# Performance work log

Measured on AMD Instinct MI355X. Metric: run time of the kernel, lower is better.

## Reference

```python
import jax, jax.numpy as jnp
import numpy as np

HIDDEN = 450
DEPTH = 8
VOCAB = 780
N_NODES = 5120
N_MESS = 10241


def setup_inputs() -> dict:
    key = jax.random.key(0)
    ks = jax.random.split(key, 16)
    s = 0.05  # weight scale for numerical sanity
    return {
        "fnode": jax.random.randint(ks[0], (N_NODES,), 0, VOCAB),
        "fmess": jax.random.randint(ks[1], (N_MESS,), 0, N_NODES),
        "node_graph": jax.random.randint(ks[2], (N_NODES, 6), 0, N_MESS),
        "mess_graph": jax.random.randint(ks[3], (N_MESS, 5), 0, N_MESS),
        "emb": jax.random.normal(ks[4], (VOCAB, HIDDEN), jnp.float32),
        "Wz": jax.random.normal(ks[5], (2 * HIDDEN, HIDDEN), jnp.float32) * s,
        "bz": jnp.zeros((HIDDEN,), jnp.float32),
        "Wr": jax.random.normal(ks[6], (HIDDEN, HIDDEN), jnp.float32) * s,
        "Ur": jax.random.normal(ks[7], (HIDDEN, HIDDEN), jnp.float32) * s,
        "bu": jnp.zeros((HIDDEN,), jnp.float32),
        "Wh": jax.random.normal(ks[8], (2 * HIDDEN, HIDDEN), jnp.float32) * s,
        "bh": jnp.zeros((HIDDEN,), jnp.float32),
        "Wo": jax.random.normal(ks[9], (2 * HIDDEN, HIDDEN), jnp.float32) * s,
        "bo": jnp.zeros((HIDDEN,), jnp.float32),
        "batch_size": 128,
    }


def _gru(fmess_e, mess_graph, Wz, bz, Wr, Ur, bu, Wh, bh):
    # JTNN graph-GRU: depth-unrolled message updates over the message graph.
    M = fmess_e.shape[0]
    h0 = jnp.zeros((M, HIDDEN), fmess_e.dtype)
    mask = jnp.ones((M, 1), fmess_e.dtype).at[0].set(0.0)  # slot 0 = dummy message
    r1 = (fmess_e @ Wr)[:, None, :]  # loop-invariant W_r(fmess), [M,1,H]

    def step(h, _):
        h_nei = h[mess_graph]                     # [M,K,H] gather (index_select_ND)
        sum_h = h_nei.sum(axis=1)                 # [M,H]
        z = jax.nn.sigmoid(jnp.concatenate([fmess_e, sum_h], -1) @ Wz + bz)
        r = jax.nn.sigmoid(r1 + h_nei @ Ur + bu)  # [M,K,H]
        sum_gh = (r * h_nei).sum(axis=1)
        pre_h = jnp.tanh(jnp.concatenate([fmess_e, sum_gh], -1) @ Wh + bh)
        h = ((1.0 - z) * sum_h + z * pre_h) * mask
        return h, None

    h, _ = jax.lax.scan(step, h0, None, length=DEPTH)
    return h


def reference(fnode, fmess, node_graph, mess_graph, emb, Wz, bz, Wr, Ur, bu,
              Wh, bh, Wo, bo, batch_size):
    x = emb[fnode]                    # [N,H] embedding gather
    fmess_e = x[fmess]                # [M,H] message input features
    h = _gru(fmess_e, mess_graph, Wz, bz, Wr, Ur, bu, Wh, bh)  # [M,H]
    mess_nei = h[node_graph]          # [N,Kn,H]
    node_vecs = jnp.concatenate([x, mess_nei.sum(axis=1)], -1)  # [N,2H]
    node_vecs = jax.nn.relu(node_vecs @ Wo + bo)                # outputNN
    # uniform scope: every tree has N_NODES // batch_size nodes -> static reshape
    tree_vecs = node_vecs.reshape(batch_size, -1, HIDDEN)       # [B,L,H]
    messages = jnp.zeros((mess_graph.shape[0], HIDDEN), node_vecs.dtype)
    return (tree_vecs, messages)
```

## Files before the change

kernel.cpp:

```cpp
#include <hip/hip_runtime.h>
#include <cstdint>
#include <cstddef>

#define H 450
#define H2 900
#define KP 480
#define KP2 960
#define NMESS 10241
#define NNODE 5120
#define MPAD 10368
#define SPP1 960
#define SPP2 1920
#define PPSZ ((size_t)MPAD * SPP1)
#define KM 5
#define KN 6
#define LDCH 960

typedef __attribute__((ext_vector_type(8))) short short8;
typedef __attribute__((ext_vector_type(4))) float f32x4;

__device__ __forceinline__ short bf16rne(float f) {
  union { float f; unsigned u; } x; x.f = f;
  unsigned u = x.u;
  u += 0x7FFF + ((u >> 16) & 1);
  return (short)(u >> 16);
}
__device__ __forceinline__ float bf16tof(short s) {
  union { float f; unsigned u; } x;
  x.u = ((unsigned)(unsigned short)s) << 16;
  return x.f;
}
__device__ __forceinline__ void bf16split(float v, short& hi, short& lo) {
  hi = bf16rne(v);
  lo = bf16rne(v - bf16tof(hi));
}
__device__ __forceinline__ float sigmoidf_(float x) {
  return 1.f / (1.f + __expf(-x));
}

__device__ __forceinline__ size_t ppix(int row, int k, int spp) {
  return (size_t)row * spp + ((k >> 5) << 6) + (k & 31);
}

__device__ __forceinline__ void gll16(const short* g, short* l) {
  __builtin_amdgcn_global_load_lds(
      (const __attribute__((address_space(1))) void*)g,
      (__attribute__((address_space(3))) void*)l, 16, 0, 0);
}

#define BM 64
#define BN 64
#define BK 32

struct SmemT { short As[2][64][64]; short Bs[2][64][64]; };

__device__ __forceinline__ void xcd_swz(int gx, int gy, int& bm, int& bn) {
  const int nwg = gx * gy;
  int lid = blockIdx.y * gx + blockIdx.x;
  const int q = nwg >> 3, r = nwg & 7;
  const int xcd = lid & 7, seq = lid >> 3;
  int sid = (xcd < r) ? (xcd * (q + 1) + seq)
                      : (r * (q + 1) + (xcd - r) * q + seq);
  bm = (sid / gx) * BM;
  bn = (sid % gx) * BN;
}

template<int ACT, int OUT>
__device__ __forceinline__ void gemm_core(
    SmemT& sm, const short* __restrict__ Apk, int Kpad,
    const short* __restrict__ Bpk,
    const float* __restrict__ bias,
    float* C, int ldc, short* Cs,
    int M, int N, int bm, int bn)
{
  const int tid  = threadIdx.x;
  const int lane = tid & 63;
  const int wid  = tid >> 6;
  const int wm   = (wid >> 1) * 32;
  const int wn   = (wid & 1) * 32;
  const int l15  = lane & 15;
  const int s8   = (lane >> 4) * 8;
  const int rr0  = (lane >> 4) * 4;
  const int spp  = Kpad * 2;

  const int lr = lane >> 3;
  const int sl = lane & 7;
  const int t0 = sl ^ lr;
  const short* src[4];
#pragma unroll
  for (int qq = 0; qq < 4; ++qq) {
    const int rrow = wid * 32 + qq * 8 + lr;
    const bool isA = rrow < 64;
    const int grow = isA ? (bm + rrow) : (bn + rrow - 64);
    src[qq] = (isA ? Apk : Bpk) + (size_t)grow * spp + t0 * 8;
  }
  const int nk = Kpad / BK;

  f32x4 acc[2][2];
#pragma unroll
  for (int i = 0; i < 2; ++i)
#pragma unroll
    for (int j = 0; j < 2; ++j)
#pragma unroll
      for (int t = 0; t < 4; ++t) acc[i][j][t] = 0.f;

  auto STAGE = [&](int b, int koff) {
#pragma unroll
    for (int qq = 0; qq < 4; ++qq) {
      const int r0 = wid * 32 + qq * 8;
      short* d = (r0 < 64) ? &sm.As[b][r0][0] : &sm.Bs[b][r0 - 64][0];
      gll16(src[qq] + koff, d);
    }
  };

  STAGE(0, 0);
  __syncthreads();
  int cur = 0;
  for (int t = 0; t < nk; ++t) {
    if (t + 1 < nk) STAGE(cur ^ 1, (t + 1) * 64);
    short8 ah[2], al[2], bh[2], bl[2];
#pragma unroll
    for (int i = 0; i < 2; ++i) {
      const int rA = wm + i*16 + l15;
      const int xr = (rA & 7) << 3;
      ah[i] = *(const short8*)&sm.As[cur][rA][(s8)      ^ xr];
      al[i] = *(const short8*)&sm.As[cur][rA][(s8 + 32) ^ xr];
    }
#pragma unroll
    for (int j = 0; j < 2; ++j) {
      const int rB = wn + j*16 + l15;
      const int xr = (rB & 7) << 3;
      bh[j] = *(const short8*)&sm.Bs[cur][rB][(s8)      ^ xr];
      bl[j] = *(const short8*)&sm.Bs[cur][rB][(s8 + 32) ^ xr];
    }
    __builtin_amdgcn_s_setprio(1);
#pragma unroll
    for (int j = 0; j < 2; ++j)
#pragma unroll
      for (int i = 0; i < 2; ++i) {
        acc[i][j] = __builtin_amdgcn_mfma_f32_16x16x32_bf16(ah[i], bh[j], acc[i][j], 0, 0, 0);
        acc[i][j] = __builtin_amdgcn_mfma_f32_16x16x32_bf16(al[i], bh[j], acc[i][j], 0, 0, 0);
        acc[i][j] = __builtin_amdgcn_mfma_f32_16x16x32_bf16(ah[i], bl[j], acc[i][j], 0, 0, 0);
      }
    __builtin_amdgcn_s_setprio(0);
    __syncthreads();
    cur ^= 1;
  }

#pragma unroll
  for (int j = 0; j < 2; ++j) {
    int col = bn + wn + j*16 + l15;
    if (col >= N) continue;
    float bv = ((OUT == 0 || OUT == 3) && bias) ? bias[col] : 0.f;
#pragma unroll
    for (int i = 0; i < 2; ++i) {
      int row0 = bm + wm + i*16 + rr0;
#pragma unroll
      for (int rr = 0; rr < 4; ++rr) {
        int row = row0 + rr;
        if (row >= M) continue;
        float v = acc[i][j][rr] + bv;
        if (OUT == 0) {
          if (ACT == 1) v = fmaxf(v, 0.f);
          C[(size_t)row * ldc + col] = v;
        } else if (OUT == 1) {
          short hi, lo; bf16split(v, hi, lo);
          size_t o = ppix(row, col, SPP1);
          Cs[o] = hi; Cs[o + 32] = lo;
        } else {
          Cs[(size_t)row * ldc + col] = bf16rne(v);
        }
      }
    }
  }
}

template<int ACT>
__global__ __launch_bounds__(256, 5)
void gemm4(const short* __restrict__ Apk, int Kpad,
           const short* __restrict__ Bpk,
           const float* __restrict__ bias,
           float* C, int ldc, int M, int N)
{
  __shared__ SmemT sm;
  int bm, bn; xcd_swz(gridDim.x, gridDim.y, bm, bn);
  gemm_core<ACT, 0>(sm, Apk, Kpad, Bpk, bias, C, ldc, nullptr, M, N, bm, bn);
}

__global__ __launch_bounds__(256, 5)
void gemm4_b(const short* __restrict__ Apk, int Kpad,
             const short* __restrict__ Bpk,
             const float* __restrict__ bias,
             short* Cs, int ldcs, int M, int N)
{
  __shared__ SmemT sm;
  int bm, bn; xcd_swz(gridDim.x, gridDim.y, bm, bn);
  gemm_core<0, 3>(sm, Apk, Kpad, Bpk, bias, nullptr, ldcs, Cs, M, N, bm, bn);
}

__global__ __launch_bounds__(256, 5)
void gemm4_pair(const short* __restrict__ A0, const short* __restrict__ B0,
                float* C0,
                const short* __restrict__ A1, const short* __restrict__ B1,
                short* C1)
{
  __shared__ SmemT sm;
  int bm, bn; xcd_swz(gridDim.x, gridDim.y, bm, bn);
  if (blockIdx.z == 0)
    gemm_core<0, 0>(sm, A0, KP, B0, nullptr, C0, H, nullptr, NMESS, H, bm, bn);
  else
    gemm_core<0, 1>(sm, A1, KP, B1, nullptr, nullptr, 0, C1, NMESS, H, bm, bn);
}

__global__ __launch_bounds__(256)
void k_wT(const float* __restrict__ W, int Kreal,
          short* __restrict__ Bt, int Kpad, int rmax) {
  __shared__ float T[32][33];
  const int tx = threadIdx.x & 31;
  const int ty = threadIdx.x >> 5;
  const int k0 = blockIdx.x * 32;
  const int c0 = blockIdx.y * 32;
  const int spp = Kpad * 2;
#pragma unroll
  for (int i = 0; i < 4; ++i) {
    int k = k0 + ty + i*8, c = c0 + tx;
    T[ty + i*8][tx] = (k < Kreal && c < H) ? W[(size_t)k * H + c] : 0.f;
  }
  __syncthreads();
#pragma unroll
  for (int i = 0; i < 4; ++i) {
    int c = c0 + ty + i*8, k = k0 + tx;
    if (k < Kpad && c < rmax) {
      short hi, lo;
      bf16split(T[tx][ty + i*8], hi, lo);
      size_t o = ppix(c, k, spp);
      Bt[o] = hi; Bt[o + 32] = lo;
    }
  }
}

__global__ void k_biascat(const float* __restrict__ bz, const float* __restrict__ bh,
                          float* __restrict__ biasI) {
  int c = blockIdx.x * blockDim.x + threadIdx.x;
  if (c >= 900) return;
  biasI[c] = (c < 450) ? bz[c] : bh[c - 450];
}


__global__ void k_build_idx(const int* __restrict__ fnode,
                            const int* __restrict__ fmess,
                            int* __restrict__ idxM) {
  int m = blockIdx.x * blockDim.x + threadIdx.x;
  if (m < NMESS) idxM[m] = fnode[fmess[m]];
}

__global__ void k_embsplit(const float* __restrict__ emb,
                           const int* __restrict__ idxM,
                           short* __restrict__ eP) {
  int m = blockIdx.x, j = threadIdx.x * 2;
  if (j >= KP) return;
  size_t o = ppix(m, j, SPP1);
  if (j < H) {
    float2 v = *(const float2*)&emb[(size_t)idxM[m] * H + j];
    short2 h2, l2;
    bf16split(v.x, h2.x, l2.x); bf16split(v.y, h2.y, l2.y);
    *(short2*)&eP[o] = h2; *(short2*)&eP[o + 32] = l2;
  } else {
    short2 z2; z2.x = 0; z2.y = 0;
    *(short2*)&eP[o] = z2; *(short2*)&eP[o + 32] = z2;
  }
}

__global__ void k_h1(const short* __restrict__ CHb, short* __restrict__ hP) {
  int m = blockIdx.x, j = threadIdx.x * 2;
  if (j >= KP) return;
  size_t oP = ppix(m, j, SPP1);
  if (j < H) {
    size_t oc = (size_t)m * LDCH + j;
    short2 cz2 = *(const short2*)&CHb[oc];
    short2 ch2 = *(const short2*)&CHb[oc + 450];
    float v0 = sigmoidf_(bf16tof(cz2.x)) * tanhf(bf16tof(ch2.x));
    float v1 = sigmoidf_(bf16tof(cz2.y)) * tanhf(bf16tof(ch2.y));
    if (m == 0) { v0 = 0.f; v1 = 0.f; }
    short2 h2, l2;
    bf16split(v0, h2.x, l2.x); bf16split(v1, h2.y, l2.y);
    *(short2*)&hP[oP] = h2; *(short2*)&hP[oP + 32] = l2;
  } else {
    short2 z2; z2.x = 0; z2.y = 0;
    *(short2*)&hP[oP] = z2; *(short2*)&hP[oP + 32] = z2;
  }
}

__global__ void k_gather2(const short* __restrict__ hP,
                          const float* __restrict__ g,
                          const short* __restrict__ r1b,
                          const int* __restrict__ mg,
                          short* __restrict__ shP, short* __restrict__ ghP) {
  int m = blockIdx.x, j = threadIdx.x * 2;
  if (j >= KP) return;
  size_t o = ppix(m, j, SPP1);
  if (j >= H) {
    short2 z2; z2.x = 0; z2.y = 0;
    *(short2*)&shP[o] = z2; *(short2*)&shP[o + 32] = z2;
    *(short2*)&ghP[o] = z2; *(short2*)&ghP[o + 32] = z2;
    return;
  }
  const int* e = mg + (size_t)m * KM;
  short2 rb2 = *(const short2*)&r1b[(size_t)m * 480 + j];
  float rb0 = bf16tof(rb2.x), rb1 = bf16tof(rb2.y);
  float s0 = 0.f, s1 = 0.f, t0 = 0.f, t1 = 0.f;
#pragma unroll
  for (int k = 0; k < KM; ++k) {
    int ek = e[k];
    size_t oP = ppix(ek, j, SPP1);
    float2 gv = *(const float2*)&g[(size_t)ek * H + j];
    short2 ph = *(const short2*)&hP[oP];
    short2 pl = *(const short2*)&hP[oP + 32];
    float h0 = bf16tof(ph.x) + bf16tof(pl.x);
    float h1 = bf16tof(ph.y) + bf16tof(pl.y);
    s0 += h0;                          s1 += h1;
    t0 += sigmoidf_(rb0 + gv.x) * h0;  t1 += sigmoidf_(rb1 + gv.y) * h1;
  }
  short2 h2, l2;
  bf16split(s0, h2.x, l2.x); bf16split(s1, h2.y, l2.y);
  *(short2*)&shP[o] = h2; *(short2*)&shP[o + 32] = l2;
  bf16split(t0, h2.x, l2.x); bf16split(t1, h2.y, l2.y);
  *(short2*)&ghP[o] = h2; *(short2*)&ghP[o + 32] = l2;
}

__global__ void k_combine(const short* __restrict__ CHb,
                          const float* __restrict__ th,
                          const short* __restrict__ shP,
                          short* hP) {
  int m = blockIdx.x, j = threadIdx.x * 2;
  if (j >= KP) return;
  size_t oP = ppix(m, j, SPP1);
  if (j >= H) {
    short2 z2; z2.x = 0; z2.y = 0;
    *(short2*)&hP[oP] = z2; *(short2*)&hP[oP + 32] = z2;
    return;
  }
  size_t oc = (size_t)m * LDCH + j;
  size_t og = (size_t)m * H + j;
  short2 cz2 = *(const short2*)&CHb[oc];
  short2 ch2 = *(const short2*)&CHb[oc + 450];
  float2 tv  = *(const float2*)&th[og];
  short2 tzh = *(const short2*)&hP[oP];
  short2 tzl = *(const short2*)&hP[oP + 32];
  short2 smh = *(const short2*)&shP[oP];
  short2 sml = *(const short2*)&shP[oP + 32];
  float tz0 = bf16tof(tzh.x) + bf16tof(tzl.x);
  float tz1 = bf16tof(tzh.y) + bf16tof(tzl.y);
  float sm0 = bf16tof(smh.x) + bf16tof(sml.x);
  float sm1 = bf16tof(smh.y) + bf16tof(sml.y);
  float z0 = sigmoidf_(bf16tof(cz2.x) + tz0);
  float z1 = sigmoidf_(bf16tof(cz2.y) + tz1);
  float p0 = tanhf(bf16tof(ch2.x) + tv.x);
  float p1 = tanhf(bf16tof(ch2.y) + tv.y);
  float v0 = (1.f - z0) * sm0 + z0 * p0;
  float v1 = (1.f - z1) * sm1 + z1 * p1;
  if (m == 0) { v0 = 0.f; v1 = 0.f; }
  short2 h2, l2;
  bf16split(v0, h2.x, l2.x); bf16split(v1, h2.y, l2.y);
  *(short2*)&hP[oP] = h2; *(short2*)&hP[oP + 32] = l2;
}

__global__ void k_nodecat(const float* __restrict__ emb,
                          const int* __restrict__ fnode,
                          const short* __restrict__ hP,
                          const int* __restrict__ ng,
                          short* __restrict__ Apk) {
  int n = blockIdx.x, t = threadIdx.x, j = t * 2;
  if (j < H) {
    float2 v = *(const float2*)&emb[(size_t)fnode[n] * H + j];
    short2 h2, l2;
    bf16split(v.x, h2.x, l2.x); bf16split(v.y, h2.y, l2.y);
    size_t o = ppix(n, j, SPP2);
    *(short2*)&Apk[o] = h2; *(short2*)&Apk[o + 32] = l2;

    const int* e = ng + (size_t)n * KN;
    float s0 = 0.f, s1 = 0.f;
#pragma unroll
    for (int k = 0; k < KN; ++k) {
      size_t oP = ppix(e[k], j, SPP1);
      short2 ph = *(const short2*)&hP[oP];
      short2 pl = *(const short2*)&hP[oP + 32];
      s0 += bf16tof(ph.x) + bf16tof(pl.x);
      s1 += bf16tof(ph.y) + bf16tof(pl.y);
    }
    bf16split(s0, h2.x, l2.x); bf16split(s1, h2.y, l2.y);
    o = ppix(n, 450 + j, SPP2);
    *(short2*)&Apk[o] = h2; *(short2*)&Apk[o + 32] = l2;
  }
  if (t < 30) {
    int c = 900 + t * 2;
    short2 z2; z2.x = 0; z2.y = 0;
    size_t o = ppix(n, c, SPP2);
    *(short2*)&Apk[o] = z2; *(short2*)&Apk[o + 32] = z2;
  }
}


extern "C" void kernel_launch(void* const* d_in, const int* in_sizes, int n_in,
                              void* d_out, int out_size, void* d_ws, size_t ws_size,
                              hipStream_t stream) {
  (void)in_sizes; (void)n_in; (void)out_size; (void)ws_size;

  const int*   fnode      = (const int*)d_in[0];
  const int*   fmess      = (const int*)d_in[1];
  const int*   node_graph = (const int*)d_in[2];
  const int*   mess_graph = (const int*)d_in[3];
  const float* emb        = (const float*)d_in[4];
  const float* Wz         = (const float*)d_in[5];
  const float* bz         = (const float*)d_in[6];
  const float* Wr         = (const float*)d_in[7];
  const float* Ur         = (const float*)d_in[8];
  const float* bu         = (const float*)d_in[9];
  const float* Wh         = (const float*)d_in[10];
  const float* bh         = (const float*)d_in[11];
  const float* Wo         = (const float*)d_in[12];
  const float* bo         = (const float*)d_in[13];

  short* P   = (short*)d_ws;
  short* hP  = P;
  short* shP = P + 1 * PPSZ;
  short* ghP = P + 2 * PPSZ;
  short* CHb = P + 3 * PPSZ;
  float* g   = (float*)(CHb + (size_t)NMESS * LDCH + 64);
  short* r1b = (short*)(g + (size_t)NMESS * H);

  char*  scr  = (char*)d_out + (size_t)NNODE * H * 4;
  short* BtI  = (short*)scr;
  short* BtR  = BtI  + (size_t)1408 * SPP1;
  short* BtUr = BtR  + (size_t)512 * SPP1;
  short* BtZ  = BtUr + (size_t)512 * SPP1;
  short* BtHH = BtZ  + (size_t)512 * SPP1;
  short* BtO  = BtHH + (size_t)512 * SPP1;
  float* biasI = (float*)(BtO + (size_t)512 * SPP2);
  int*   idxM  = (int*)(biasI + 912);

  k_build_idx<<<(NMESS + 255) / 256, 256, 0, stream>>>(fnode, fmess, idxM);

  dim3 gT(KP / 32, 16), gT2(KP2 / 32, 16);
  k_wT<<<gT,  256, 0, stream>>>(Wz,                  H, BtI,               KP,  512);
  k_wT<<<gT,  256, 0, stream>>>(Wh,                  H, BtI + 450 * SPP1,  KP,  512);
  k_wT<<<gT,  256, 0, stream>>>(Wr,                  H, BtR,               KP,  512);
  k_wT<<<gT,  256, 0, stream>>>(Ur,                  H, BtUr,              KP,  512);
  k_wT<<<gT,  256, 0, stream>>>(Wz + (size_t)H * H,  H, BtZ,               KP,  512);
  k_wT<<<gT,  256, 0, stream>>>(Wh + (size_t)H * H,  H, BtHH,              KP,  512);
  k_wT<<<gT2, 256, 0, stream>>>(Wo,                 H2, BtO,               KP2, 512);
  k_biascat<<<4, 256, 0, stream>>>(bz, bh, biasI);

  k_embsplit<<<NMESS, 256, 0, stream>>>(emb, idxM, ghP);

  dim3 gI1(15, MPAD / BM);
  gemm4_b<<<gI1, 256, 0, stream>>>(ghP, KP, BtI, biasI, CHb, LDCH, NMESS, H2);
  dim3 gI2(8, MPAD / BM);
  gemm4_b<<<gI2, 256, 0, stream>>>(ghP, KP, BtR, bu, r1b, 480, NMESS, H);

  k_h1<<<NMESS, 256, 0, stream>>>(CHb, hP);

  dim3 gB(8, MPAD / BM);
  dim3 gP(8, MPAD / BM, 2);
  for (int d = 1; d < 8; ++d) {
    gemm4<0><<<gB, 256, 0, stream>>>(hP, KP, BtUr, nullptr, g, H, NMESS, H);
    k_gather2<<<NMESS, 256, 0, stream>>>(hP, g, r1b, mess_graph, shP, ghP);
    gemm4_pair<<<gP, 256, 0, stream>>>(ghP, BtHH, g, shP, BtZ, hP);
    k_combine<<<NMESS, 256, 0, stream>>>(CHb, g, shP, hP);
  }

  k_nodecat<<<NNODE, 256, 0, stream>>>(emb, fnode, hP, node_graph, shP);
  dim3 gF(8, NNODE / BM);
  gemm4<1><<<gF, 256, 0, stream>>>(shP, KP2, BtO, bo, (float*)d_out, H, NNODE, H);

  hipMemsetAsync((float*)d_out + (size_t)NNODE * H, 0, (size_t)NMESS * H * sizeof(float), stream);
}
```

Measured before the change: 902.8 us.

## Use linearity to compute Z-gate from per-message h@Wz, fuse combine into GEMM epilogue

```diff
diff --git a/kernel.cpp b/kernel.cpp
--- a/kernel.cpp
+++ b/kernel.cpp
@@ -71,6 +71,8 @@
     const short* __restrict__ Bpk,
     const float* __restrict__ bias,
     float* C, int ldc, short* Cs,
+    const short* __restrict__ E1, const short* __restrict__ E2,
+    const short* __restrict__ E3,
     int M, int N, int bm, int bn)
 {
   const int tid  = threadIdx.x;
@@ -163,12 +165,20 @@
         if (OUT == 0) {
           if (ACT == 1) v = fmaxf(v, 0.f);
           C[(size_t)row * ldc + col] = v;
-        } else if (OUT == 1) {
-          short hi, lo; bf16split(v, hi, lo);
-          size_t o = ppix(row, col, SPP1);
-          Cs[o] = hi; Cs[o + 32] = lo;
+        } else if (OUT == 3) {
+          Cs[(size_t)row * ldc + col] = bf16rne(v);
         } else {
-          Cs[(size_t)row * ldc + col] = bf16rne(v);
+          float tz = bf16tof(E2[(size_t)row * 480 + col]);
+          float cz = bf16tof(E1[(size_t)row * LDCH + col]);
+          float ch = bf16tof(E1[(size_t)row * LDCH + 450 + col]);
+          size_t op = ppix(row, col, SPP1);
+          float sm2 = bf16tof(E3[op]) + bf16tof(E3[op + 32]);
+          float z   = sigmoidf_(cz + tz);
+          float pre = tanhf(ch + v);
+          float hv  = (1.f - z) * sm2 + z * pre;
+          if (row == 0) hv = 0.f;
+          short hi, lo; bf16split(hv, hi, lo);
+          Cs[op] = hi; Cs[op + 32] = lo;
         }
       }
     }
@@ -184,7 +194,8 @@
 {
   __shared__ SmemT sm;
   int bm, bn; xcd_swz(gridDim.x, gridDim.y, bm, bn);
-  gemm_core<ACT, 0>(sm, Apk, Kpad, Bpk, bias, C, ldc, nullptr, M, N, bm, bn);
+  gemm_core<ACT, 0>(sm, Apk, Kpad, Bpk, bias, C, ldc, nullptr,
+                    nullptr, nullptr, nullptr, M, N, bm, bn);
 }
 
 __global__ __launch_bounds__(256, 5)
@@ -195,21 +206,22 @@
 {
   __shared__ SmemT sm;
   int bm, bn; xcd_swz(gridDim.x, gridDim.y, bm, bn);
-  gemm_core<0, 3>(sm, Apk, Kpad, Bpk, bias, nullptr, ldcs, Cs, M, N, bm, bn);
+  gemm_core<0, 3>(sm, Apk, Kpad, Bpk, bias, nullptr, ldcs, Cs,
+                  nullptr, nullptr, nullptr, M, N, bm, bn);
 }
 
 __global__ __launch_bounds__(256, 5)
-void gemm4_pair(const short* __restrict__ A0, const short* __restrict__ B0,
-                float* C0,
-                const short* __restrict__ A1, const short* __restrict__ B1,
-                short* C1)
+void gemm4_thc(const short* __restrict__ Apk,
+               const short* __restrict__ Bpk,
+               const short* __restrict__ CHb,
+               const short* __restrict__ tzb,
+               const short* __restrict__ shP,
+               short* hP)
 {
   __shared__ SmemT sm;
   int bm, bn; xcd_swz(gridDim.x, gridDim.y, bm, bn);
-  if (blockIdx.z == 0)
-    gemm_core<0, 0>(sm, A0, KP, B0, nullptr, C0, H, nullptr, NMESS, H, bm, bn);
-  else
-    gemm_core<0, 1>(sm, A1, KP, B1, nullptr, nullptr, 0, C1, NMESS, H, bm, bn);
+  gemm_core<0, 4>(sm, Apk, KP, Bpk, nullptr, nullptr, 0, hP,
+                  CHb, tzb, shP, NMESS, H, bm, bn);
 }
 
 __global__ __launch_bounds__(256)
@@ -291,11 +303,12 @@
   }
 }
 
-__global__ void k_gather2(const short* __restrict__ hP,
-                          const float* __restrict__ g,
+__global__ void k_gather3(const short* __restrict__ hP,
+                          const short* __restrict__ GU,
                           const short* __restrict__ r1b,
                           const int* __restrict__ mg,
-                          short* __restrict__ shP, short* __restrict__ ghP) {
+                          short* __restrict__ shP, short* __restrict__ ghP,
+                          short* __restrict__ tzb) {
   int m = blockIdx.x, j = threadIdx.x * 2;
   if (j >= KP) return;
   size_t o = ppix(m, j, SPP1);
@@ -308,61 +321,29 @@
   const int* e = mg + (size_t)m * KM;
   short2 rb2 = *(const short2*)&r1b[(size_t)m * 480 + j];
   float rb0 = bf16tof(rb2.x), rb1 = bf16tof(rb2.y);
-  float s0 = 0.f, s1 = 0.f, t0 = 0.f, t1 = 0.f;
+  float s0 = 0.f, s1 = 0.f, t0 = 0.f, t1 = 0.f, u0 = 0.f, u1 = 0.f;
 #pragma unroll
   for (int k = 0; k < KM; ++k) {
     int ek = e[k];
     size_t oP = ppix(ek, j, SPP1);
-    float2 gv = *(const float2*)&g[(size_t)ek * H + j];
+    size_t oG = (size_t)ek * LDCH + j;
+    short2 gv = *(const short2*)&GU[oG];
+    short2 uv = *(const short2*)&GU[oG + 450];
     short2 ph = *(const short2*)&hP[oP];
     short2 pl = *(const short2*)&hP[oP + 32];
     float h0 = bf16tof(ph.x) + bf16tof(pl.x);
     float h1 = bf16tof(ph.y) + bf16tof(pl.y);
-    s0 += h0;                          s1 += h1;
-    t0 += sigmoidf_(rb0 + gv.x) * h0;  t1 += sigmoidf_(rb1 + gv.y) * h1;
+    s0 += h0;                                  s1 += h1;
+    t0 += sigmoidf_(rb0 + bf16tof(gv.x)) * h0; t1 += sigmoidf_(rb1 + bf16tof(gv.y)) * h1;
+    u0 += bf16tof(uv.x);                       u1 += bf16tof(uv.y);
   }
   short2 h2, l2;
   bf16split(s0, h2.x, l2.x); bf16split(s1, h2.y, l2.y);
   *(short2*)&shP[o] = h2; *(short2*)&shP[o + 32] = l2;
   bf16split(t0, h2.x, l2.x); bf16split(t1, h2.y, l2.y);
   *(short2*)&ghP[o] = h2; *(short2*)&ghP[o + 32] = l2;
-}
-
-__global__ void k_combine(const short* __restrict__ CHb,
-                          const float* __restrict__ th,
-                          const short* __restrict__ shP,
-                          short* hP) {
-  int m = blockIdx.x, j = threadIdx.x * 2;
-  if (j >= KP) return;
-  size_t oP = ppix(m, j, SPP1);
-  if (j >= H) {
-    short2 z2; z2.x = 0; z2.y = 0;
-    *(short2*)&hP[oP] = z2; *(short2*)&hP[oP + 32] = z2;
-    return;
-  }
-  size_t oc = (size_t)m * LDCH + j;
-  size_t og = (size_t)m * H + j;
-  short2 cz2 = *(const short2*)&CHb[oc];
-  short2 ch2 = *(const short2*)&CHb[oc + 450];
-  float2 tv  = *(const float2*)&th[og];
-  short2 tzh = *(const short2*)&hP[oP];
-  short2 tzl = *(const short2*)&hP[oP + 32];
-  short2 smh = *(const short2*)&shP[oP];
-  short2 sml = *(const short2*)&shP[oP + 32];
-  float tz0 = bf16tof(tzh.x) + bf16tof(tzl.x);
-  float tz1 = bf16tof(tzh.y) + bf16tof(tzl.y);
-  float sm0 = bf16tof(smh.x) + bf16tof(sml.x);
-  float sm1 = bf16tof(smh.y) + bf16tof(sml.y);
-  float z0 = sigmoidf_(bf16tof(cz2.x) + tz0);
-  float z1 = sigmoidf_(bf16tof(cz2.y) + tz1);
-  float p0 = tanhf(bf16tof(ch2.x) + tv.x);
-  float p1 = tanhf(bf16tof(ch2.y) + tv.y);
-  float v0 = (1.f - z0) * sm0 + z0 * p0;
-  float v1 = (1.f - z1) * sm1 + z1 * p1;
-  if (m == 0) { v0 = 0.f; v1 = 0.f; }
-  short2 h2, l2;
-  bf16split(v0, h2.x, l2.x); bf16split(v1, h2.y, l2.y);
-  *(short2*)&hP[oP] = h2; *(short2*)&hP[oP + 32] = l2;
+  short2 tz2; tz2.x = bf16rne(u0); tz2.y = bf16rne(u1);
+  *(short2*)&tzb[(size_t)m * 480 + j] = tz2;
 }
 
 __global__ void k_nodecat(const float* __restrict__ emb,
@@ -426,15 +407,15 @@
   short* shP = P + 1 * PPSZ;
   short* ghP = P + 2 * PPSZ;
   short* CHb = P + 3 * PPSZ;
-  float* g   = (float*)(CHb + (size_t)NMESS * LDCH + 64);
-  short* r1b = (short*)(g + (size_t)NMESS * H);
+  short* GU  = CHb + (size_t)NMESS * LDCH;
+  short* r1b = GU  + (size_t)NMESS * LDCH;
+  short* tzb = r1b + (size_t)NMESS * 480;
 
   char*  scr  = (char*)d_out + (size_t)NNODE * H * 4;
   short* BtI  = (short*)scr;
   short* BtR  = BtI  + (size_t)1408 * SPP1;
-  short* BtUr = BtR  + (size_t)512 * SPP1;
-  short* BtZ  = BtUr + (size_t)512 * SPP1;
-  short* BtHH = BtZ  + (size_t)512 * SPP1;
+  short* BtGU = BtR  + (size_t)512 * SPP1;
+  short* BtHH = BtGU + (size_t)1024 * SPP1;
   short* BtO  = BtHH + (size_t)512 * SPP1;
   float* biasI = (float*)(BtO + (size_t)512 * SPP2);
   int*   idxM  = (int*)(biasI + 912);
@@ -445,8 +426,8 @@
   k_wT<<<gT,  256, 0, stream>>>(Wz,                  H, BtI,               KP,  512);
   k_wT<<<gT,  256, 0, stream>>>(Wh,                  H, BtI + 450 * SPP1,  KP,  512);
   k_wT<<<gT,  256, 0, stream>>>(Wr,                  H, BtR,               KP,  512);
-  k_wT<<<gT,  256, 0, stream>>>(Ur,                  H, BtUr,              KP,  512);
-  k_wT<<<gT,  256, 0, stream>>>(Wz + (size_t)H * H,  H, BtZ,               KP,  512);
+  k_wT<<<gT,  256, 0, stream>>>(Ur,                  H, BtGU,              KP,  512);
+  k_wT<<<gT,  256, 0, stream>>>(Wz + (size_t)H * H,  H, BtGU + 450 * SPP1, KP,  512);
   k_wT<<<gT,  256, 0, stream>>>(Wh + (size_t)H * H,  H, BtHH,              KP,  512);
   k_wT<<<gT2, 256, 0, stream>>>(Wo,                 H2, BtO,               KP2, 512);
   k_biascat<<<4, 256, 0, stream>>>(bz, bh, biasI);
@@ -460,13 +441,12 @@
 
   k_h1<<<NMESS, 256, 0, stream>>>(CHb, hP);
 
+  dim3 gGU(15, MPAD / BM);
   dim3 gB(8, MPAD / BM);
-  dim3 gP(8, MPAD / BM, 2);
   for (int d = 1; d < 8; ++d) {
-    gemm4<0><<<gB, 256, 0, stream>>>(hP, KP, BtUr, nullptr, g, H, NMESS, H);
-    k_gather2<<<NMESS, 256, 0, stream>>>(hP, g, r1b, mess_graph, shP, ghP);
-    gemm4_pair<<<gP, 256, 0, stream>>>(ghP, BtHH, g, shP, BtZ, hP);
-    k_combine<<<NMESS, 256, 0, stream>>>(CHb, g, shP, hP);
+    gemm4_b<<<gGU, 256, 0, stream>>>(hP, KP, BtGU, nullptr, GU, LDCH, NMESS, H2);
+    k_gather3<<<NMESS, 256, 0, stream>>>(hP, GU, r1b, mess_graph, shP, ghP, tzb);
+    gemm4_thc<<<gB, 256, 0, stream>>>(ghP, BtHH, CHb, tzb, shP, hP);
   }
 
   k_nodecat<<<NNODE, 256, 0, stream>>>(emb, fnode, hP, node_graph, shP);
```

Result: slower. 937.4 us (+3.8%).
